# Performance work log

Hardware: AMD Instinct MI355X
Metric: run time of the kernel (lower is better)

## Reference

```python
import jax, jax.numpy as jnp
import numpy as np

EPS = 1e-5
GROUPS = 32

def group_norm(x, gamma, beta):
    B, C, H, W = x.shape
    g = x.reshape(B, GROUPS, C // GROUPS, H, W)
    mu = g.mean(axis=(2, 3, 4), keepdims=True)
    var = g.var(axis=(2, 3, 4), keepdims=True)
    g = (g - mu) * jax.lax.rsqrt(var + EPS)
    x = g.reshape(B, C, H, W)
    return x * gamma[None, :, None, None] + beta[None, :, None, None]

def setup_inputs() -> dict:
    key = jax.random.key(0)
    ks = jax.random.split(key, 6)
    C = 512
    x = jax.random.normal(ks[0], (16, C, 32, 32), dtype=jnp.float32)
    gamma = jnp.ones((C,), jnp.float32)
    beta = jnp.zeros((C,), jnp.float32)
    w_qkv = jax.random.normal(ks[1], (3 * C, C), jnp.float32) / np.sqrt(C)
    b_qkv = jnp.zeros((3 * C,), jnp.float32)
    w_proj = jax.random.normal(ks[2], (C, C), jnp.float32) / np.sqrt(C)
    b_proj = jnp.zeros((C,), jnp.float32)
    return {"x": x, "gamma": gamma, "beta": beta, "w_qkv": w_qkv,
            "b_qkv": b_qkv, "w_proj": w_proj, "b_proj": b_proj}

def reference(x, gamma, beta, w_qkv, b_qkv, w_proj, b_proj):
    B, C, H, W = x.shape
    h = group_norm(x, gamma, beta)
    # 1x1 conv == per-pixel linear over channels
    qkv = jnp.einsum('bchw,oc->bohw', h, w_qkv) + b_qkv[None, :, None, None]
    q, k, v = jnp.split(qkv, 3, axis=1)
    N = H * W
    q = q.reshape(B, C, N)            # [B,C,N]
    k = k.reshape(B, C, N)
    v = v.reshape(B, C, N)
    attn = jnp.einsum('bci,bcj->bij', q, k) / jnp.sqrt(jnp.float32(C))
    attn = jax.nn.softmax(attn, axis=-1)          # [B,N,N]
    out = jnp.einsum('bij,bcj->bci', attn, v)     # [B,C,N]
    out = out.reshape(B, C, H, W)
    out = jnp.einsum('bchw,oc->bohw', out, w_proj) + b_proj[None, :, None, None]
    return x + out
```

## Files before the change

kernel.cpp:

```cpp
#include <hip/hip_runtime.h>
#include <hip/hip_bf16.h>

#define BATCH 16
#define CH    512
#define NPIX  1024
#define GRP   32
#define CPG   16

typedef __attribute__((ext_vector_type(8))) short bf16x8;
typedef __attribute__((ext_vector_type(4))) float f32x4;

__device__ __forceinline__ ushort f2b(float f) {
    union { float f; unsigned u; } v; v.f = f;
    unsigned u = v.u;
    u += 0x7FFF + ((u >> 16) & 1);
    return (ushort)(u >> 16);
}

#define GLD16(gp, lp) __builtin_amdgcn_global_load_lds( \
    (__attribute__((address_space(1))) void*)(gp), \
    (__attribute__((address_space(3))) void*)(lp), 16, 0, 0)

__global__ __launch_bounds__(256) void convert_weights(
    const float* __restrict__ wq, const float* __restrict__ wp,
    ushort* __restrict__ wq_b, ushort* __restrict__ wp_b,
    float* __restrict__ rowsum) {
    int i = blockIdx.x * 256 + threadIdx.x;
    if (i < 786432) wq_b[i] = f2b(wq[i]);
    else            wp_b[i - 786432] = f2b(wp[i - 786432]);
    if (i < BATCH * NPIX) rowsum[i] = 0.f;
}

__global__ __launch_bounds__(256) void gn_stats(
    const float* __restrict__ x, float* __restrict__ mu, float* __restrict__ rs) {
    int g = blockIdx.x, b = blockIdx.y;
    const float4* p = (const float4*)(x + ((size_t)b * CH + g * CPG) * NPIX);
    float s = 0.f, ss = 0.f;
    for (int i = threadIdx.x; i < 4096; i += 256) {
        float4 v = p[i];
        s  += v.x + v.y + v.z + v.w;
        ss += v.x*v.x + v.y*v.y + v.z*v.z + v.w*v.w;
    }
    for (int o = 1; o < 64; o <<= 1) { s += __shfl_xor(s, o); ss += __shfl_xor(ss, o); }
    __shared__ float as[4], bs[4];
    int w = threadIdx.x >> 6;
    if ((threadIdx.x & 63) == 0) { as[w] = s; bs[w] = ss; }
    __syncthreads();
    if (threadIdx.x == 0) {
        s  = as[0] + as[1] + as[2] + as[3];
        ss = bs[0] + bs[1] + bs[2] + bs[3];
        float m = s * (1.0f / 16384.0f);
        float var = ss * (1.0f / 16384.0f) - m * m;
        mu[b * GRP + g] = m;
        rs[b * GRP + g] = rsqrtf(var + 1e-5f);
    }
}

__global__ __launch_bounds__(256) void gn_norm_t(
    const float* __restrict__ x, const float* __restrict__ mu, const float* __restrict__ rs,
    const float* __restrict__ gamma, const float* __restrict__ beta, ushort* __restrict__ hT) {
    int c0 = blockIdx.x * 32, n0 = blockIdx.y * 128, b = blockIdx.z;
    __shared__ ushort t[128 * 32];
    int tid = threadIdx.x;
#pragma unroll
    for (int i = 0; i < 4; i++) {
        int f = tid + i * 256;
        int c = f >> 5, nf = f & 31;
        int cg = c0 + c;
        float m = mu[b * GRP + (cg >> 4)], r = rs[b * GRP + (cg >> 4)];
        float ga = gamma[cg] * r;
        float be = beta[cg] - m * ga;
        float4 v = *(const float4*)(x + ((size_t)(b * CH + cg)) * NPIX + n0 + nf * 4);
        float vv[4] = {v.x, v.y, v.z, v.w};
#pragma unroll
        for (int j = 0; j < 4; j++) {
            int n = nf * 4 + j;
            int pos = (c >> 3) ^ ((n >> 2) & 3);
            t[n * 32 + pos * 8 + (c & 7)] = f2b(vv[j] * ga + be);
        }
    }
    __syncthreads();
#pragma unroll
    for (int i = 0; i < 2; i++) {
        int ch = tid + i * 256;
        int n = ch >> 2, g = ch & 3;
        int pos = g ^ ((n >> 2) & 3);
        uint4 val = *(const uint4*)&t[n * 32 + pos * 8];
        *(uint4*)(hT + ((size_t)b * NPIX + n0 + n) * CH + c0 + g * 8) = val;
    }
}

#define BK 64

template<int EPI, int BMt, int BNt>
__global__ __launch_bounds__(256, 4) void gemm_bt(
    const ushort* __restrict__ A, long sA, int lda,
    const ushort* __restrict__ Bt, long sB, int ldb,
    int K,
    void* __restrict__ Out, long sO, int ldo,
    const float* __restrict__ bias,
    const float* __restrict__ resid,
    ushort* __restrict__ vout,
    float* __restrict__ rowsum,
    float scale) {
    constexpr int FM = BMt / 32;
    constexpr int FN = BNt / 32;
    constexpr int SA = BMt / 32;
    constexpr int SB = BNt / 32;
    __shared__ __align__(16) ushort sh[(BMt + BNt) * BK];
    ushort* As = sh;
    ushort* Bs = sh + BMt * BK;
    int b = blockIdx.z;
    A  += (size_t)b * sA;
    Bt += (size_t)b * sB;
    int m0 = blockIdx.y * BMt, n0 = blockIdx.x * BNt;
    int tid = threadIdx.x;
    int lane = tid & 63;
    int wave = tid >> 6;
    int q = lane >> 4, l = lane & 15;
    int wm = (wave >> 1) * (BMt / 2), wn = (wave & 1) * (BNt / 2);

    int aoff[SA], boff[SB], lofa[SA], lofb[SB];
#pragma unroll
    for (int i = 0; i < SA; i++) {
        int p = tid + i * 256, r = p >> 3, g = (p & 7) ^ (r & 7);
        aoff[i] = (m0 + r) * lda + g * 8;
        lofa[i] = p * 8;
    }
#pragma unroll
    for (int i = 0; i < SB; i++) {
        int p = tid + i * 256, r = p >> 3, g = (p & 7) ^ (r & 7);
        boff[i] = (n0 + r) * ldb + g * 8;
        lofb[i] = p * 8;
    }

    int offA[FM][2], offB[FN][2];
#pragma unroll
    for (int mi = 0; mi < FM; mi++) {
        int r = wm + mi * 16 + l;
#pragma unroll
        for (int kk = 0; kk < 2; kk++)
            offA[mi][kk] = r * 64 + ((((kk << 2) | q) ^ (r & 7)) * 8);
    }
#pragma unroll
    for (int ni = 0; ni < FN; ni++) {
        int r = wn + ni * 16 + l;
#pragma unroll
        for (int kk = 0; kk < 2; kk++)
            offB[ni][kk] = r * 64 + ((((kk << 2) | q) ^ (r & 7)) * 8);
    }

    f32x4 zero = {0.f, 0.f, 0.f, 0.f};
    f32x4 acc[FM][FN];
#pragma unroll
    for (int mi = 0; mi < FM; mi++)
#pragma unroll
        for (int ni = 0; ni < FN; ni++) acc[mi][ni] = zero;

    for (int k0 = 0; k0 < K; k0 += BK) {
        __syncthreads();
#pragma unroll
        for (int i = 0; i < SA; i++) GLD16(A + aoff[i] + k0, As + lofa[i]);
#pragma unroll
        for (int i = 0; i < SB; i++) GLD16(Bt + boff[i] + k0, Bs + lofb[i]);
        __syncthreads();
#pragma unroll
        for (int kk = 0; kk < 2; kk++) {
            bf16x8 af[FM], bfr[FN];
#pragma unroll
            for (int mi = 0; mi < FM; mi++) af[mi]  = *(const bf16x8*)(As + offA[mi][kk]);
#pragma unroll
            for (int ni = 0; ni < FN; ni++) bfr[ni] = *(const bf16x8*)(Bs + offB[ni][kk]);
#pragma unroll
            for (int mi = 0; mi < FM; mi++)
#pragma unroll
                for (int ni = 0; ni < FN; ni++)
                    acc[mi][ni] = __builtin_amdgcn_mfma_f32_16x16x32_bf16(
                        af[mi], bfr[ni], acc[mi][ni], 0, 0, 0);
        }
    }

    if (EPI == 0) {
        if (n0 >= 1024) {
            __syncthreads();
#pragma unroll
            for (int mi = 0; mi < FM; mi++)
#pragma unroll
                for (int ni = 0; ni < FN; ni++) {
                    int nl = wn + ni * 16 + l;
                    float bi = bias[n0 + nl];
#pragma unroll
                    for (int rg = 0; rg < 4; rg++) {
                        int ml = wm + mi * 16 + q * 4 + rg;
                        int pos = (ml >> 3) ^ (nl & 15);
                        sh[nl * 128 + pos * 8 + (ml & 7)] = f2b(acc[mi][ni][rg] + bi);
                    }
                }
            __syncthreads();
#pragma unroll
            for (int i = 0; i < 8; i++) {
                int idx = tid + i * 256;
                int nl = idx >> 4, ch = idx & 15;
                int g2 = ch ^ (nl & 15);
                uint4 val = *(const uint4*)&sh[nl * 128 + g2 * 8];
                *(uint4*)(vout + (size_t)b * (512 * 1024)
                          + (size_t)(n0 - 1024 + nl) * 1024 + m0 + ch * 8) = val;
            }
            return;
        }
#pragma unroll
        for (int mi = 0; mi < FM; mi++)
#pragma unroll
            for (int ni = 0; ni < FN; ni++) {
                int n = n0 + wn + ni * 16 + l;
                float bi = bias[n];
#pragma unroll
                for (int rg = 0; rg < 4; rg++) {
                    int m = m0 + wm + mi * 16 + q * 4 + rg;
                    ((ushort*)Out)[(size_t)b * sO + (size_t)m * ldo + n] =
                        f2b(acc[mi][ni][rg] + bi);
                }
            }
        return;
    }
    if (EPI == 1) {
#pragma unroll
        for (int mi = 0; mi < FM; mi++) {
            float rsum[4] = {0.f, 0.f, 0.f, 0.f};
#pragma unroll
            for (int ni = 0; ni < FN; ni++) {
                int n = n0 + wn + ni * 16 + l;
#pragma unroll
                for (int rg = 0; rg < 4; rg++) {
                    int m = m0 + wm + mi * 16 + q * 4 + rg;
                    float u = __expf(acc[mi][ni][rg] * scale);
                    rsum[rg] += u;
                    ((ushort*)Out)[(size_t)b * sO + (size_t)m * ldo + n] = f2b(u);
                }
            }
#pragma unroll
            for (int rg = 0; rg < 4; rg++) {
                float s = rsum[rg];
                s += __shfl_xor(s, 1); s += __shfl_xor(s, 2);
                s += __shfl_xor(s, 4); s += __shfl_xor(s, 8);
                if (l == 0)
                    atomicAdd(&rowsum[b * NPIX + m0 + wm + mi * 16 + q * 4 + rg], s);
            }
        }
        return;
    }
#pragma unroll
    for (int mi = 0; mi < FM; mi++) {
        float inv[4];
        if (EPI == 2) {
#pragma unroll
            for (int rg = 0; rg < 4; rg++)
                inv[rg] = 1.0f / rowsum[b * NPIX + m0 + wm + mi * 16 + q * 4 + rg];
        }
#pragma unroll
        for (int ni = 0; ni < FN; ni++) {
            int mbase = m0 + wm + mi * 16 + q * 4;
            int n = n0 + wn + ni * 16 + l;
#pragma unroll
            for (int rg = 0; rg < 4; rg++) {
                int m = mbase + rg;
                float v = acc[mi][ni][rg];
                if (EPI == 2) {
                    ((ushort*)Out)[(size_t)b * sO + (size_t)m * ldo + n] = f2b(v * inv[rg]);
                } else {
                    v += bias[m] + resid[(size_t)b * sO + (size_t)m * ldo + n];
                    ((float*)Out)[(size_t)b * sO + (size_t)m * ldo + n] = v;
                }
            }
        }
    }
}

extern "C" void kernel_launch(void* const* d_in, const int* in_sizes, int n_in,
                              void* d_out, int out_size, void* d_ws, size_t ws_size,
                              hipStream_t stream) {
    const float* x     = (const float*)d_in[0];
    const float* gamma = (const float*)d_in[1];
    const float* beta  = (const float*)d_in[2];
    const float* wqkv  = (const float*)d_in[3];
    const float* bqkv  = (const float*)d_in[4];
    const float* wproj = (const float*)d_in[5];
    const float* bproj = (const float*)d_in[6];
    float* out = (float*)d_out;
    char* ws = (char*)d_ws;

    ushort* wq_b   = (ushort*)(ws + 0);
    ushort* wp_b   = (ushort*)(ws + 1572864);
    float*  mu     = (float*)(ws + 2097152);
    float*  rs     = (float*)(ws + 2099200);
    float*  rowsum = (float*)(ws + 2101248);
    ushort* hT     = (ushort*)(ws + 2166784);
    ushort* qk     = (ushort*)(ws + 18944000);
    ushort* vb     = (ushort*)(ws + 52498432);
    ushort* u      = (ushort*)(ws + 69275648);
    ushort* O1T    = hT;

    convert_weights<<<4096, 256, 0, stream>>>(wqkv, wproj, wq_b, wp_b, rowsum);
    gn_stats<<<dim3(GRP, BATCH), 256, 0, stream>>>(x, mu, rs);
    gn_norm_t<<<dim3(16, 8, BATCH), 256, 0, stream>>>(x, mu, rs, gamma, beta, hT);

    gemm_bt<0, 128, 128><<<dim3(12, 8, BATCH), 256, 0, stream>>>(
        hT, 524288, 512, wq_b, 0, 512, 512,
        qk, 1048576, 1024, bqkv, nullptr, vb, nullptr, 0.f);

    gemm_bt<1, 128, 128><<<dim3(8, 8, BATCH), 256, 0, stream>>>(
        qk, 1048576, 1024, qk + 512, 1048576, 1024, 512,
        u, 1048576, 1024, nullptr, nullptr, nullptr, rowsum, 0.044194173824159216f);

    gemm_bt<2, 128, 64><<<dim3(8, 8, BATCH), 256, 0, stream>>>(
        u, 1048576, 1024, vb, 524288, 1024, 1024,
        O1T, 524288, 512, nullptr, nullptr, nullptr, rowsum, 0.f);

    gemm_bt<3, 64, 128><<<dim3(8, 8, BATCH), 256, 0, stream>>>(
        wp_b, 0, 512, O1T, 524288, 512, 512,
        out, 524288, 1024, bproj, x, nullptr, nullptr, 0.f);
}
```

Measured before the change: 239.2 us.

## Fuse QK^T, softmax and PV into a single flash-style attention kernel

Replaces the two attention GEMM launches, which wrote the full unnormalized exp(QK^T) matrix to global memory and accumulated row sums with atomics, with one fused kernel. Each block holds a 32-row Q tile in LDS, streams K in 64-column chunks, stages exp scores in LDS and multiplies them with V, then normalizes by the row sums at the end. This removes the 32 MB score buffer round-trip, the atomics and the rowsum zeroing. It still skips max subtraction, as the old code did, and it reads K and V straight from global memory without LDS staging, with only 512 blocks and high register use that may limit occupancy.

```diff
diff --git a/kernel.cpp b/kernel.cpp
--- a/kernel.cpp
+++ b/kernel.cpp
@@ -21,14 +21,14 @@
     (__attribute__((address_space(1))) void*)(gp), \
     (__attribute__((address_space(3))) void*)(lp), 16, 0, 0)
 
+#define MFMA(a, b, c) __builtin_amdgcn_mfma_f32_16x16x32_bf16(a, b, c, 0, 0, 0)
+
 __global__ __launch_bounds__(256) void convert_weights(
     const float* __restrict__ wq, const float* __restrict__ wp,
-    ushort* __restrict__ wq_b, ushort* __restrict__ wp_b,
-    float* __restrict__ rowsum) {
+    ushort* __restrict__ wq_b, ushort* __restrict__ wp_b) {
     int i = blockIdx.x * 256 + threadIdx.x;
     if (i < 786432) wq_b[i] = f2b(wq[i]);
     else            wp_b[i - 786432] = f2b(wp[i - 786432]);
-    if (i < BATCH * NPIX) rowsum[i] = 0.f;
 }
 
 __global__ __launch_bounds__(256) void gn_stats(
@@ -90,6 +90,121 @@
     }
 }
 
+#define QT 32
+#define JT 64
+
+__global__ __launch_bounds__(256, 2) void attn_fused(
+    const ushort* __restrict__ qk, const ushort* __restrict__ vb,
+    ushort* __restrict__ O1T, float scale) {
+    __shared__ __align__(16) ushort qs[QT * 512];
+    __shared__ __align__(16) ushort ps[QT * JT];
+    __shared__ float rsbuf[2][QT];
+    int flat = blockIdx.x;
+    int xcd = flat & 7, idx = flat >> 3;
+    int b = xcd * 2 + (idx & 1);
+    int m0 = (idx >> 1) * QT;
+    const ushort* qkb = qk + (size_t)b * (NPIX * 1024);
+    const ushort* vbb = vb + (size_t)b * (CH * NPIX);
+    int tid = threadIdx.x, lane = tid & 63, wave = tid >> 6;
+    int q = lane >> 4, l = lane & 15;
+    int wm = (wave >> 1) * 16, wn = (wave & 1) * 32;
+    int cslice = wave * 128;
+
+#pragma unroll
+    for (int i = 0; i < 8; i++) {
+        int s = tid + i * 256, r = s >> 6, pos = s & 63;
+        int G = (pos & ~7) | ((pos & 7) ^ (r & 7));
+        GLD16(qkb + (size_t)(m0 + r) * 1024 + G * 8, qs + s * 8);
+    }
+
+    const ushort* qbe = qs + (wm + l) * 512 + ((q ^ (l & 7)) * 8);
+    const ushort* qbo = qs + (wm + l) * 512 + (((q | 4) ^ (l & 7)) * 8);
+    const ushort* pb00 = ps + l * 64 + ((q ^ (l & 7)) * 8);
+    const ushort* pb01 = ps + l * 64 + (((4 + q) ^ (l & 7)) * 8);
+    const ushort* pb10 = pb00 + 16 * 64;
+    const ushort* pb11 = pb01 + 16 * 64;
+    const ushort* pv[8];
+#pragma unroll
+    for (int ni = 0; ni < 8; ni++)
+        pv[ni] = vbb + (size_t)(cslice + ni * 16 + l) * 1024 + q * 8;
+
+    float rs[4] = {0.f, 0.f, 0.f, 0.f};
+    f32x4 zero = {0.f, 0.f, 0.f, 0.f};
+    f32x4 oacc[2][8];
+#pragma unroll
+    for (int mi = 0; mi < 2; mi++)
+#pragma unroll
+        for (int ni = 0; ni < 8; ni++) oacc[mi][ni] = zero;
+
+    __syncthreads();
+
+    for (int jc = 0; jc < 16; jc++) {
+        int j0 = jc * 64;
+        f32x4 sacc0 = zero, sacc1 = zero;
+        const ushort* pk0 = qkb + (size_t)(j0 + wn + l) * 1024 + 512 + q * 8;
+        const ushort* pk1 = pk0 + 16 * 1024;
+#pragma unroll
+        for (int t = 0; t < 16; t++) {
+            bf16x8 a = *(const bf16x8*)(((t & 1) ? qbo : qbe) + (t >> 1) * 64);
+            bf16x8 b0 = *(const bf16x8*)(pk0 + t * 32);
+            bf16x8 b1 = *(const bf16x8*)(pk1 + t * 32);
+            sacc0 = MFMA(a, b0, sacc0);
+            sacc1 = MFMA(a, b1, sacc1);
+        }
+#pragma unroll
+        for (int rg = 0; rg < 4; rg++) {
+            int row = wm + q * 4 + rg;
+            float u0 = __expf(sacc0[rg] * scale);
+            float u1 = __expf(sacc1[rg] * scale);
+            rs[rg] += u0 + u1;
+            int c0i = wn + l, c1i = wn + 16 + l;
+            ps[row * 64 + (((c0i >> 3) ^ (row & 7)) * 8) + (c0i & 7)] = f2b(u0);
+            ps[row * 64 + (((c1i >> 3) ^ (row & 7)) * 8) + (c1i & 7)] = f2b(u1);
+        }
+        __syncthreads();
+#pragma unroll
+        for (int kk = 0; kk < 2; kk++) {
+            bf16x8 pa0 = *(const bf16x8*)((kk ? pb01 : pb00));
+            bf16x8 pa1 = *(const bf16x8*)((kk ? pb11 : pb10));
+#pragma unroll
+            for (int ni = 0; ni < 8; ni++) {
+                bf16x8 vv = *(const bf16x8*)(pv[ni] + j0 + kk * 32);
+                oacc[0][ni] = MFMA(pa0, vv, oacc[0][ni]);
+                oacc[1][ni] = MFMA(pa1, vv, oacc[1][ni]);
+            }
+        }
+        __syncthreads();
+    }
+
+#pragma unroll
+    for (int rg = 0; rg < 4; rg++) {
+        float s = rs[rg];
+        s += __shfl_xor(s, 1); s += __shfl_xor(s, 2);
+        s += __shfl_xor(s, 4); s += __shfl_xor(s, 8);
+        if (l == 0) rsbuf[wave & 1][wm + q * 4 + rg] = s;
+    }
+    __syncthreads();
+
+#pragma unroll
+    for (int mi = 0; mi < 2; mi++) {
+        float inv[4];
+#pragma unroll
+        for (int rg = 0; rg < 4; rg++) {
+            int r = mi * 16 + q * 4 + rg;
+            inv[rg] = 1.0f / (rsbuf[0][r] + rsbuf[1][r]);
+        }
+#pragma unroll
+        for (int ni = 0; ni < 8; ni++) {
+            int c = cslice + ni * 16 + l;
+#pragma unroll
+            for (int rg = 0; rg < 4; rg++) {
+                int i = m0 + mi * 16 + q * 4 + rg;
+                O1T[((size_t)b * NPIX + i) * CH + c] = f2b(oacc[mi][ni][rg] * inv[rg]);
+            }
+        }
+    }
+}
+
 #define BK 64
 
 template<int EPI, int BMt, int BNt>
@@ -101,7 +216,6 @@
     const float* __restrict__ bias,
     const float* __restrict__ resid,
     ushort* __restrict__ vout,
-    float* __restrict__ rowsum,
     float scale) {
     constexpr int FM = BMt / 32;
     constexpr int FN = BNt / 32;
@@ -175,8 +289,7 @@
             for (int mi = 0; mi < FM; mi++)
 #pragma unroll
                 for (int ni = 0; ni < FN; ni++)
-                    acc[mi][ni] = __builtin_amdgcn_mfma_f32_16x16x32_bf16(
-                        af[mi], bfr[ni], acc[mi][ni], 0, 0, 0);
+                    acc[mi][ni] = MFMA(af[mi], bfr[ni], acc[mi][ni]);
         }
     }
 
@@ -223,40 +336,8 @@
             }
         return;
     }
-    if (EPI == 1) {
-#pragma unroll
-        for (int mi = 0; mi < FM; mi++) {
-            float rsum[4] = {0.f, 0.f, 0.f, 0.f};
-#pragma unroll
-            for (int ni = 0; ni < FN; ni++) {
-                int n = n0 + wn + ni * 16 + l;
-#pragma unroll
-                for (int rg = 0; rg < 4; rg++) {
-                    int m = m0 + wm + mi * 16 + q * 4 + rg;
-                    float u = __expf(acc[mi][ni][rg] * scale);
-                    rsum[rg] += u;
-                    ((ushort*)Out)[(size_t)b * sO + (size_t)m * ldo + n] = f2b(u);
-                }
-            }
-#pragma unroll
-            for (int rg = 0; rg < 4; rg++) {
-                float s = rsum[rg];
-                s += __shfl_xor(s, 1); s += __shfl_xor(s, 2);
-                s += __shfl_xor(s, 4); s += __shfl_xor(s, 8);
-                if (l == 0)
-                    atomicAdd(&rowsum[b * NPIX + m0 + wm + mi * 16 + q * 4 + rg], s);
-            }
-        }
-        return;
-    }
-#pragma unroll
-    for (int mi = 0; mi < FM; mi++) {
-        float inv[4];
-        if (EPI == 2) {
-#pragma unroll
-            for (int rg = 0; rg < 4; rg++)
-                inv[rg] = 1.0f / rowsum[b * NPIX + m0 + wm + mi * 16 + q * 4 + rg];
-        }
+#pragma unroll
+    for (int mi = 0; mi < FM; mi++)
 #pragma unroll
         for (int ni = 0; ni < FN; ni++) {
             int mbase = m0 + wm + mi * 16 + q * 4;
@@ -264,16 +345,10 @@
 #pragma unroll
             for (int rg = 0; rg < 4; rg++) {
                 int m = mbase + rg;
-                float v = acc[mi][ni][rg];
-                if (EPI == 2) {
-                    ((ushort*)Out)[(size_t)b * sO + (size_t)m * ldo + n] = f2b(v * inv[rg]);
-                } else {
-                    v += bias[m] + resid[(size_t)b * sO + (size_t)m * ldo + n];
-                    ((float*)Out)[(size_t)b * sO + (size_t)m * ldo + n] = v;
-                }
-            }
-        }
-    }
+                float v = acc[mi][ni][rg] + bias[m] + resid[(size_t)b * sO + (size_t)m * ldo + n];
+                ((float*)Out)[(size_t)b * sO + (size_t)m * ldo + n] = v;
+            }
+        }
 }
 
 extern "C" void kernel_launch(void* const* d_in, const int* in_sizes, int n_in,
@@ -293,30 +368,22 @@
     ushort* wp_b   = (ushort*)(ws + 1572864);
     float*  mu     = (float*)(ws + 2097152);
     float*  rs     = (float*)(ws + 2099200);
-    float*  rowsum = (float*)(ws + 2101248);
-    ushort* hT     = (ushort*)(ws + 2166784);
-    ushort* qk     = (ushort*)(ws + 18944000);
-    ushort* vb     = (ushort*)(ws + 52498432);
-    ushort* u      = (ushort*)(ws + 69275648);
+    ushort* hT     = (ushort*)(ws + 2101248);
+    ushort* qk     = (ushort*)(ws + 18878464);
+    ushort* vb     = (ushort*)(ws + 52432896);
     ushort* O1T    = hT;
 
-    convert_weights<<<4096, 256, 0, stream>>>(wqkv, wproj, wq_b, wp_b, rowsum);
+    convert_weights<<<4096, 256, 0, stream>>>(wqkv, wproj, wq_b, wp_b);
     gn_stats<<<dim3(GRP, BATCH), 256, 0, stream>>>(x, mu, rs);
     gn_norm_t<<<dim3(16, 8, BATCH), 256, 0, stream>>>(x, mu, rs, gamma, beta, hT);
 
     gemm_bt<0, 128, 128><<<dim3(12, 8, BATCH), 256, 0, stream>>>(
         hT, 524288, 512, wq_b, 0, 512, 512,
-        qk, 1048576, 1024, bqkv, nullptr, vb, nullptr, 0.f);
-
-    gemm_bt<1, 128, 128><<<dim3(8, 8, BATCH), 256, 0, stream>>>(
-        qk, 1048576, 1024, qk + 512, 1048576, 1024, 512,
-        u, 1048576, 1024, nullptr, nullptr, nullptr, rowsum, 0.044194173824159216f);
-
-    gemm_bt<2, 128, 64><<<dim3(8, 8, BATCH), 256, 0, stream>>>(
-        u, 1048576, 1024, vb, 524288, 1024, 1024,
-        O1T, 524288, 512, nullptr, nullptr, nullptr, rowsum, 0.f);
+        qk, 1048576, 1024, bqkv, nullptr, vb, 0.f);
+
+    attn_fused<<<512, 256, 0, stream>>>(qk, vb, O1T, 0.044194173824159216f);
 
     gemm_bt<3, 64, 128><<<dim3(8, 8, BATCH), 256, 0, stream>>>(
         wp_b, 0, 512, O1T, 524288, 512, 512,
-        out, 524288, 1024, bproj, x, nullptr, nullptr, 0.f);
-}
+        out, 524288, 1024, bproj, x, nullptr, 0.f);
+}
```

After: 350.4 us. +46.5%, slower.
